# Performance work log

Measured on AMD Instinct MI355X. Metric: run time of the kernel, lower is better.

## Reference

```python
import jax, jax.numpy as jnp
import numpy as np

N_NODES = 500_000
N_EDGES = 16_000_000
GCN_DIMS = [1, 4, 7, 10, 16]   # gcn layer in/out widths
MLP_DIMS = [16, 32, 16, 16]    # fc1, fc2, fc3 (raw_feature_size=16)


def setup_inputs() -> dict:
    key = jax.random.key(0)
    ks = list(jax.random.split(key, 40))
    ki = iter(ks)
    inp = {}
    inp["x"] = jax.random.normal(next(ki), (N_NODES, 1), dtype=jnp.float32)
    inp["edge_index"] = jax.random.randint(next(ki), (2, N_EDGES), 0, N_NODES, dtype=jnp.int32)
    # GraphConv params: lin_rel (weight+bias) applied to aggregated neighbors,
    # lin_root (weight, no bias) applied to self features.
    for li in range(4):
        din, dout = GCN_DIMS[li], GCN_DIMS[li + 1]
        s = 1.0 / np.sqrt(din)
        inp[f"g{li+1}_Wrel"] = jax.random.uniform(next(ki), (din, dout), jnp.float32, -s, s)
        inp[f"g{li+1}_brel"] = jax.random.uniform(next(ki), (dout,), jnp.float32, -s, s)
        inp[f"g{li+1}_Wroot"] = jax.random.uniform(next(ki), (din, dout), jnp.float32, -s, s)
    for li in range(3):
        din, dout = MLP_DIMS[li], MLP_DIMS[li + 1]
        s = 1.0 / np.sqrt(din)
        inp[f"fc{li+1}_W"] = jax.random.uniform(next(ki), (din, dout), jnp.float32, -s, s)
        inp[f"fc{li+1}_b"] = jax.random.uniform(next(ki), (dout,), jnp.float32, -s, s)
    return inp


def _graph_conv(x, Wrel, brel, Wroot, src, dst):
    # PyG GraphConv, aggr='add': out_i = Wrel @ (sum_{j->i} x_j) + brel + Wroot @ x_i
    agg = jax.ops.segment_sum(x[src], dst, num_segments=N_NODES)  # [N, din]
    return agg @ Wrel + brel + x @ Wroot


def reference(x, edge_index,
              g1_Wrel, g1_brel, g1_Wroot,
              g2_Wrel, g2_brel, g2_Wroot,
              g3_Wrel, g3_brel, g3_Wroot,
              g4_Wrel, g4_brel, g4_Wroot,
              fc1_W, fc1_b, fc2_W, fc2_b, fc3_W, fc3_b):
    src, dst = edge_index[0], edge_index[1]
    h = jax.nn.relu(_graph_conv(x, g1_Wrel, g1_brel, g1_Wroot, src, dst))
    h = jax.nn.relu(_graph_conv(h, g2_Wrel, g2_brel, g2_Wroot, src, dst))
    h = jax.nn.relu(_graph_conv(h, g3_Wrel, g3_brel, g3_Wroot, src, dst))
    h = jax.nn.relu(_graph_conv(h, g4_Wrel, g4_brel, g4_Wroot, src, dst))
    h = jax.nn.relu(h @ fc1_W + fc1_b)
    h = jax.nn.relu(h @ fc2_W + fc2_b)
    return h @ fc3_W + fc3_b
```

## Files before the change

### kernel.cpp

```cpp
#include <hip/hip_runtime.h>
#include <hip/hip_fp16.h>

#define N_NODES 500000
#define N_EDGES 16000000

#define SB_BITS 13
#define SB_SIZE (1 << SB_BITS)
#define NSUPER ((N_NODES + SB_SIZE - 1) / SB_SIZE)
#define CAP1 270336
#define BKT_BITS 9
#define BKT_SIZE (1 << BKT_BITS)
#define NBUCKET ((N_NODES + BKT_SIZE - 1) / BKT_SIZE)
#define BKT_CAP 18432
#define B1_EPT 256
#define B1_CHUNK (256 * B1_EPT)
#define B1_NBLK ((N_EDGES + B1_CHUNK - 1) / B1_CHUNK)
#define B1_VQ (B1_EPT / 4)
#define NV4 (N_EDGES / 4)
#define B2_PER_SUPER 8

typedef unsigned int u32x2 __attribute__((ext_vector_type(2)));
typedef unsigned int u32x4 __attribute__((ext_vector_type(4)));
typedef float f32x2 __attribute__((ext_vector_type(2)));
typedef float f32x4 __attribute__((ext_vector_type(4)));

__device__ __forceinline__ unsigned int h2u(__half2 h) { return *(unsigned int*)&h; }
__device__ __forceinline__ float2 u2f2(unsigned int u) { return __half22float2(*(__half2*)&u); }

__global__ __launch_bounds__(512) void init_bcur_kernel(
    int* __restrict__ bcur1, int* __restrict__ bcur2)
{
    int i = blockIdx.x * 512 + threadIdx.x;
    if (i < NSUPER) bcur1[i] = i * CAP1;
    if (i < NBUCKET) bcur2[i] = i * BKT_CAP;
}

__global__ __launch_bounds__(256) void bin1_kernel(
    const int* __restrict__ src, const int* __restrict__ dst,
    int* __restrict__ bcur1, unsigned int* __restrict__ pairs1)
{
    __shared__ int lh[NSUPER];
    __shared__ int lbase[NSUPER];
    const int4* dst4 = (const int4*)dst;
    const int4* src4 = (const int4*)src;
    int t = threadIdx.x;
    long v0 = (long)blockIdx.x * (B1_CHUNK / 4);

    if (t < NSUPER) lh[t] = 0;
    __syncthreads();

#pragma unroll 8
    for (int q = 0; q < B1_VQ; ++q) {
        long v = v0 + q * 256 + t;
        if (v < NV4) {
            int4 d = dst4[v];
            atomicAdd(&lh[d.x >> SB_BITS], 1);
            atomicAdd(&lh[d.y >> SB_BITS], 1);
            atomicAdd(&lh[d.z >> SB_BITS], 1);
            atomicAdd(&lh[d.w >> SB_BITS], 1);
        }
    }
    __syncthreads();

    if (t < NSUPER) {
        int c = lh[t];
        lbase[t] = c ? atomicAdd(&bcur1[t], c) : 0;
        lh[t] = 0;
    }
    __syncthreads();

#pragma unroll 8
    for (int q = 0; q < B1_VQ; ++q) {
        long v = v0 + q * 256 + t;
        if (v < NV4) {
            int4 d = dst4[v];
            int4 s = src4[v];
            {
                int b = d.x >> SB_BITS;
                int r = atomicAdd(&lh[b], 1);
                pairs1[lbase[b] + r] = ((unsigned int)s.x << SB_BITS) | (unsigned int)(d.x & (SB_SIZE - 1));
            }
            {
                int b = d.y >> SB_BITS;
                int r = atomicAdd(&lh[b], 1);
                pairs1[lbase[b] + r] = ((unsigned int)s.y << SB_BITS) | (unsigned int)(d.y & (SB_SIZE - 1));
            }
            {
                int b = d.z >> SB_BITS;
                int r = atomicAdd(&lh[b], 1);
                pairs1[lbase[b] + r] = ((unsigned int)s.z << SB_BITS) | (unsigned int)(d.z & (SB_SIZE - 1));
            }
            {
                int b = d.w >> SB_BITS;
                int r = atomicAdd(&lh[b], 1);
                pairs1[lbase[b] + r] = ((unsigned int)s.w << SB_BITS) | (unsigned int)(d.w & (SB_SIZE - 1));
            }
        }
    }
}

__global__ __launch_bounds__(256) void bin2_kernel(
    const int* __restrict__ bcur1, int* __restrict__ bcur2,
    const unsigned int* __restrict__ pairs1, unsigned int* __restrict__ pairs2)
{
    __shared__ int lh[16];
    __shared__ int lbase[16];
    int s = blockIdx.x >> 3;
    int blk = blockIdx.x & 7;
    int t = threadIdx.x;
    int count = bcur1[s] - s * CAP1;
    int chunk = (((count + B2_PER_SUPER - 1) / B2_PER_SUPER) + 3) & ~3;
    int lo = blk * chunk;
    int hi = lo + chunk; if (hi > count) hi = count;
    int len = hi > lo ? hi - lo : 0;
    const unsigned int* base = pairs1 + (size_t)s * CAP1 + lo;
    const uint4* p4 = (const uint4*)base;
    int nv = len >> 2;

    if (t < 16) lh[t] = 0;
    __syncthreads();

    for (int i = t; i < nv; i += 256) {
        uint4 p = p4[i];
        atomicAdd(&lh[(p.x & (SB_SIZE - 1)) >> BKT_BITS], 1);
        atomicAdd(&lh[(p.y & (SB_SIZE - 1)) >> BKT_BITS], 1);
        atomicAdd(&lh[(p.z & (SB_SIZE - 1)) >> BKT_BITS], 1);
        atomicAdd(&lh[(p.w & (SB_SIZE - 1)) >> BKT_BITS], 1);
    }
    if (t < (len & 3))
        atomicAdd(&lh[(base[(nv << 2) + t] & (SB_SIZE - 1)) >> BKT_BITS], 1);
    __syncthreads();

    if (t < 16) {
        int c = lh[t];
        lbase[t] = c ? atomicAdd(&bcur2[(s << 4) | t], c) : 0;
        lh[t] = 0;
    }
    __syncthreads();

    for (int i = t; i < nv; i += 256) {
        uint4 p = p4[i];
#pragma unroll
        for (int q = 0; q < 4; ++q) {
            unsigned int e = (q == 0) ? p.x : (q == 1) ? p.y : (q == 2) ? p.z : p.w;
            int sub = (int)((e & (SB_SIZE - 1)) >> BKT_BITS);
            int r = atomicAdd(&lh[sub], 1);
            pairs2[lbase[sub] + r] = ((e >> SB_BITS) << BKT_BITS) | (e & (BKT_SIZE - 1));
        }
    }
    if (t < (len & 3)) {
        unsigned int e = base[(nv << 2) + t];
        int sub = (int)((e & (SB_SIZE - 1)) >> BKT_BITS);
        int r = atomicAdd(&lh[sub], 1);
        pairs2[lbase[sub] + r] = ((e >> SB_BITS) << BKT_BITS) | (e & (BKT_SIZE - 1));
    }
}

__global__ __launch_bounds__(512) void bucket_scan_kernel(
    const int* __restrict__ bcur2, int* __restrict__ bbase)
{
    __shared__ int sdata[512];
    int t = threadIdx.x;
    int i0 = t * 2;
    int v0 = (i0 < NBUCKET) ? (bcur2[i0] - i0 * BKT_CAP) : 0;
    int v1 = (i0 + 1 < NBUCKET) ? (bcur2[i0 + 1] - (i0 + 1) * BKT_CAP) : 0;
    int s = v0 + v1;
    sdata[t] = s;
    __syncthreads();
    for (int o = 1; o < 512; o <<= 1) {
        int tmp = (t >= o) ? sdata[t - o] : 0;
        __syncthreads();
        sdata[t] += tmp;
        __syncthreads();
    }
    int run = sdata[t] - s;
    if (i0 < NBUCKET) bbase[i0] = run;
    if (i0 + 1 < NBUCKET) bbase[i0 + 1] = run + v0;
    if (i0 == NBUCKET - 1) bbase[NBUCKET] = run + v0;
    if (i0 + 1 == NBUCKET - 1) bbase[NBUCKET] = run + v0 + v1;
}

__global__ __launch_bounds__(512) void bucket_sort512_kernel(
    const int* __restrict__ bcur2, const int* __restrict__ bbase,
    const unsigned int* __restrict__ pairs2, const float* __restrict__ xfeat,
    int* __restrict__ off, int* __restrict__ sorted_src,
    float* __restrict__ agg1)
{
    __shared__ int   stage[BKT_CAP];
    __shared__ int   lh[BKT_SIZE];
    __shared__ float laccum[BKT_SIZE];
    __shared__ int   sdata[512];
    int b = blockIdx.x;
    int t = threadIdx.x;
    int base_node = b << BKT_BITS;
    size_t pstart = (size_t)b * BKT_CAP;
    int count = bcur2[b] - b * BKT_CAP;
    int cstart = bbase[b];

    lh[t] = 0; laccum[t] = 0.0f;
    __syncthreads();

    int nv = count >> 2;
    const uint4* p4 = (const uint4*)(pairs2 + pstart);
    for (int i = t; i < nv; i += 512) {
        uint4 p = p4[i];
        atomicAdd(&lh[p.x & (BKT_SIZE - 1)], 1);
        atomicAdd(&lh[p.y & (BKT_SIZE - 1)], 1);
        atomicAdd(&lh[p.z & (BKT_SIZE - 1)], 1);
        atomicAdd(&lh[p.w & (BKT_SIZE - 1)], 1);
    }
    if (t < (count & 3))
        atomicAdd(&lh[pairs2[pstart + (nv << 2) + t] & (BKT_SIZE - 1)], 1);
    __syncthreads();

    int c = lh[t];
    sdata[t] = c;
    __syncthreads();
    for (int o = 1; o < 512; o <<= 1) {
        int tmp = (t >= o) ? sdata[t - o] : 0;
        __syncthreads();
        sdata[t] += tmp;
        __syncthreads();
    }
    int run = cstart + sdata[t] - c;
    int node = base_node + t;
    if (node < N_NODES) {
        off[node] = run;
        if (node == N_NODES - 1) off[N_NODES] = run + c;
    }
    lh[t] = run;
    __syncthreads();

    for (int i = t; i < nv; i += 512) {
        uint4 p = p4[i];
#pragma unroll
        for (int q = 0; q < 4; ++q) {
            unsigned int pe = (q == 0) ? p.x : (q == 1) ? p.y : (q == 2) ? p.z : p.w;
            int low = (int)(pe & (BKT_SIZE - 1));
            int sidx = (int)(pe >> BKT_BITS);
            int pos = atomicAdd(&lh[low], 1);
            stage[pos - cstart] = sidx;
            atomicAdd(&laccum[low], xfeat[sidx]);
        }
    }
    if (t < (count & 3)) {
        unsigned int pe = pairs2[pstart + (nv << 2) + t];
        int low = (int)(pe & (BKT_SIZE - 1));
        int sidx = (int)(pe >> BKT_BITS);
        int pos = atomicAdd(&lh[low], 1);
        stage[pos - cstart] = sidx;
        atomicAdd(&laccum[low], xfeat[sidx]);
    }
    __syncthreads();

    for (int j = t; j < count; j += 512)
        __builtin_nontemporal_store(stage[j], &sorted_src[cstart + j]);
    if (node < N_NODES) __builtin_nontemporal_store(laccum[t], &agg1[node]);
}

__global__ __launch_bounds__(256) void transform1_kernel(
    const float* __restrict__ agg1, const float* __restrict__ x,
    const float* __restrict__ Wrel, const float* __restrict__ brel,
    const float* __restrict__ Wroot,
    __half2* __restrict__ h1)
{
    __shared__ float w[12];
    if (threadIdx.x < 4) {
        w[threadIdx.x] = Wrel[threadIdx.x];
        w[4 + threadIdx.x] = brel[threadIdx.x];
        w[8 + threadIdx.x] = Wroot[threadIdx.x];
    }
    __syncthreads();
    int i = blockIdx.x * blockDim.x + threadIdx.x;
    if (i >= N_NODES) return;
    float a = agg1[i], xv = x[i];
    float r0 = fmaxf(a * w[0] + w[4] + xv * w[8],  0.0f);
    float r1 = fmaxf(a * w[1] + w[5] + xv * w[9],  0.0f);
    float r2 = fmaxf(a * w[2] + w[6] + xv * w[10], 0.0f);
    float r3 = fmaxf(a * w[3] + w[7] + xv * w[11], 0.0f);
    u32x2 v = { h2u(__floats2half2_rn(r0, r1)), h2u(__floats2half2_rn(r2, r3)) };
    __builtin_nontemporal_store(v, (u32x2*)(h1 + (size_t)i * 2));
}

__global__ __launch_bounds__(256) void gather2t_kernel(
    const int* __restrict__ off, const int* __restrict__ ss,
    const __half2* __restrict__ h1,
    const float* __restrict__ Wrel, const float* __restrict__ brel,
    const float* __restrict__ Wroot,
    __half2* __restrict__ h2)
{
    __shared__ float tile[128 * 5];
    __shared__ float sWr[28], sWo[28], sb[7];
    int t = threadIdx.x;
    if (t < 28) { sWr[t] = Wrel[t]; sWo[t] = Wroot[t]; }
    if (t < 7) sb[t] = brel[t];

    int ln = t >> 1;
    int j = t & 1;
    int node = blockIdx.x * 128 + ln;
    if (node < N_NODES) {
        int start = off[node], end = off[node + 1];
        float a0x=0,a0y=0,a1x=0,a1y=0,a2x=0,a2y=0,a3x=0,a3y=0;
        float b0x=0,b0y=0,b1x=0,b1y=0,b2x=0,b2y=0,b3x=0,b3y=0;
        int e = start;
        for (; e + 8 <= end; e += 8) {
            int s0=ss[e],s1=ss[e+1],s2=ss[e+2],s3=ss[e+3];
            int s4=ss[e+4],s5=ss[e+5],s6=ss[e+6],s7=ss[e+7];
            float2 f0=__half22float2(h1[(size_t)s0*2+j]);
            float2 f1=__half22float2(h1[(size_t)s1*2+j]);
            float2 f2=__half22float2(h1[(size_t)s2*2+j]);
            float2 f3=__half22float2(h1[(size_t)s3*2+j]);
            float2 f4=__half22float2(h1[(size_t)s4*2+j]);
            float2 f5=__half22float2(h1[(size_t)s5*2+j]);
            float2 f6=__half22float2(h1[(size_t)s6*2+j]);
            float2 f7=__half22float2(h1[(size_t)s7*2+j]);
            a0x+=f0.x;a0y+=f0.y; a1x+=f1.x;a1y+=f1.y;
            a2x+=f2.x;a2y+=f2.y; a3x+=f3.x;a3y+=f3.y;
            b0x+=f4.x;b0y+=f4.y; b1x+=f5.x;b1y+=f5.y;
            b2x+=f6.x;b2y+=f6.y; b3x+=f7.x;b3y+=f7.y;
        }
        for (; e < end; ++e) {
            float2 f = __half22float2(h1[(size_t)ss[e]*2+j]);
            a0x += f.x; a0y += f.y;
        }
        float rx = ((a0x+a1x)+(a2x+a3x)) + ((b0x+b1x)+(b2x+b3x));
        float ry = ((a0y+a1y)+(a2y+a3y)) + ((b0y+b1y)+(b2y+b3y));
        tile[ln * 5 + 2 * j] = rx;
        tile[ln * 5 + 2 * j + 1] = ry;
    }
    __syncthreads();

    if (t < 128) {
        int n2 = blockIdx.x * 128 + t;
        if (n2 < N_NODES) {
            float av[4];
#pragma unroll
            for (int k = 0; k < 4; ++k) av[k] = tile[t * 5 + k];
            float2 x01 = __half22float2(h1[(size_t)n2 * 2]);
            float2 x23 = __half22float2(h1[(size_t)n2 * 2 + 1]);
            float xv[4] = {x01.x, x01.y, x23.x, x23.y};
            float o_[8];
#pragma unroll
            for (int o = 0; o < 7; ++o) {
                float v = sb[o];
#pragma unroll
                for (int k = 0; k < 4; ++k)
                    v += av[k] * sWr[k * 7 + o] + xv[k] * sWo[k * 7 + o];
                o_[o] = fmaxf(v, 0.0f);
            }
            o_[7] = 0.0f;
            u32x4 v = { h2u(__floats2half2_rn(o_[0], o_[1])),
                        h2u(__floats2half2_rn(o_[2], o_[3])),
                        h2u(__floats2half2_rn(o_[4], o_[5])),
                        h2u(__floats2half2_rn(o_[6], o_[7])) };
            __builtin_nontemporal_store(v, (u32x4*)(h2 + (size_t)n2 * 4));
        }
    }
}

__global__ __launch_bounds__(256) void gather3t_kernel(
    const int* __restrict__ off, const int* __restrict__ ss,
    const __half2* __restrict__ h2,
    const float* __restrict__ Wrel, const float* __restrict__ brel,
    const float* __restrict__ Wroot,
    __half2* __restrict__ h3)
{
    __shared__ float tile[64 * 9];
    __shared__ float sWr[70], sWo[70], sb[10];
    int t = threadIdx.x;
    if (t < 70) { sWr[t] = Wrel[t]; sWo[t] = Wroot[t]; }
    if (t < 10) sb[t] = brel[t];

    int ln = t >> 2;
    int j = t & 3;
    int node = blockIdx.x * 64 + ln;
    if (node < N_NODES) {
        int start = off[node], end = off[node + 1];
        float a0x=0,a0y=0,a1x=0,a1y=0,a2x=0,a2y=0,a3x=0,a3y=0;
        float b0x=0,b0y=0,b1x=0,b1y=0,b2x=0,b2y=0,b3x=0,b3y=0;
        int e = start;
        for (; e + 8 <= end; e += 8) {
            int s0=ss[e],s1=ss[e+1],s2=ss[e+2],s3=ss[e+3];
            int s4=ss[e+4],s5=ss[e+5],s6=ss[e+6],s7=ss[e+7];
            float2 f0=__half22float2(h2[(size_t)s0*4+j]);
            float2 f1=__half22float2(h2[(size_t)s1*4+j]);
            float2 f2=__half22float2(h2[(size_t)s2*4+j]);
            float2 f3=__half22float2(h2[(size_t)s3*4+j]);
            float2 f4=__half22float2(h2[(size_t)s4*4+j]);
            float2 f5=__half22float2(h2[(size_t)s5*4+j]);
            float2 f6=__half22float2(h2[(size_t)s6*4+j]);
            float2 f7=__half22float2(h2[(size_t)s7*4+j]);
            a0x+=f0.x;a0y+=f0.y; a1x+=f1.x;a1y+=f1.y;
            a2x+=f2.x;a2y+=f2.y; a3x+=f3.x;a3y+=f3.y;
            b0x+=f4.x;b0y+=f4.y; b1x+=f5.x;b1y+=f5.y;
            b2x+=f6.x;b2y+=f6.y; b3x+=f7.x;b3y+=f7.y;
        }
        for (; e < end; ++e) {
            float2 f = __half22float2(h2[(size_t)ss[e]*4+j]);
            a0x += f.x; a0y += f.y;
        }
        float rx = ((a0x+a1x)+(a2x+a3x)) + ((b0x+b1x)+(b2x+b3x));
        float ry = ((a0y+a1y)+(a2y+a3y)) + ((b0y+b1y)+(b2y+b3y));
        tile[ln * 9 + 2 * j] = rx;
        tile[ln * 9 + 2 * j + 1] = ry;
    }
    __syncthreads();

    if (t < 64) {
        int n2 = blockIdx.x * 64 + t;
        if (n2 < N_NODES) {
            float av[7];
#pragma unroll
            for (int k = 0; k < 7; ++k) av[k] = tile[t * 9 + k];
            float xv[8];
#pragma unroll
            for (int q = 0; q < 4; ++q) {
                float2 f = __half22float2(h2[(size_t)n2 * 4 + q]);
                xv[2 * q] = f.x; xv[2 * q + 1] = f.y;
            }
            float o_[16];
#pragma unroll
            for (int o = 0; o < 10; ++o) {
                float v = sb[o];
#pragma unroll
                for (int k = 0; k < 7; ++k)
                    v += av[k] * sWr[k * 10 + o] + xv[k] * sWo[k * 10 + o];
                o_[o] = fmaxf(v, 0.0f);
            }
#pragma unroll
            for (int o = 10; o < 16; ++o) o_[o] = 0.0f;
            u32x4 v0 = { h2u(__floats2half2_rn(o_[0], o_[1])),
                         h2u(__floats2half2_rn(o_[2], o_[3])),
                         h2u(__floats2half2_rn(o_[4], o_[5])),
                         h2u(__floats2half2_rn(o_[6], o_[7])) };
            u32x4 v1 = { h2u(__floats2half2_rn(o_[8], o_[9])),
                         h2u(__floats2half2_rn(o_[10], o_[11])),
                         h2u(__floats2half2_rn(o_[12], o_[13])),
                         h2u(__floats2half2_rn(o_[14], o_[15])) };
            __builtin_nontemporal_store(v0, (u32x4*)(h3 + (size_t)n2 * 8));
            __builtin_nontemporal_store(v1, (u32x4*)(h3 + (size_t)n2 * 8 + 4));
        }
    }
}

__global__ __launch_bounds__(256) void gather4_kernel(
    const int* __restrict__ off, const int* __restrict__ ss,
    const __half2* __restrict__ h3, float* __restrict__ agg)
{
    int node = blockIdx.x * 32 + (threadIdx.x >> 3);
    int j = threadIdx.x & 7;
    if (node >= N_NODES) return;
    int start = off[node], end = off[node + 1];

    float a0x=0,a0y=0,a1x=0,a1y=0,a2x=0,a2y=0,a3x=0,a3y=0;
    float b0x=0,b0y=0,b1x=0,b1y=0,b2x=0,b2y=0,b3x=0,b3y=0;
    int e = start;
    for (; e + 16 <= end; e += 16) {
        int s0=ss[e+0], s1=ss[e+1], s2=ss[e+2],  s3=ss[e+3];
        int s4=ss[e+4], s5=ss[e+5], s6=ss[e+6],  s7=ss[e+7];
        int s8=ss[e+8], s9=ss[e+9], sa=ss[e+10], sb=ss[e+11];
        int sc=ss[e+12],sd=ss[e+13],se=ss[e+14], sf=ss[e+15];
        float2 f0=__half22float2(h3[(size_t)s0*8+j]);
        float2 f1=__half22float2(h3[(size_t)s1*8+j]);
        float2 f2=__half22float2(h3[(size_t)s2*8+j]);
        float2 f3=__half22float2(h3[(size_t)s3*8+j]);
        float2 f4=__half22float2(h3[(size_t)s4*8+j]);
        float2 f5=__half22float2(h3[(size_t)s5*8+j]);
        float2 f6=__half22float2(h3[(size_t)s6*8+j]);
        float2 f7=__half22float2(h3[(size_t)s7*8+j]);
        float2 f8=__half22float2(h3[(size_t)s8*8+j]);
        float2 f9=__half22float2(h3[(size_t)s9*8+j]);
        float2 fa=__half22float2(h3[(size_t)sa*8+j]);
        float2 fb=__half22float2(h3[(size_t)sb*8+j]);
        float2 fc=__half22float2(h3[(size_t)sc*8+j]);
        float2 fd=__half22float2(h3[(size_t)sd*8+j]);
        float2 fe=__half22float2(h3[(size_t)se*8+j]);
        float2 ff=__half22float2(h3[(size_t)sf*8+j]);
        a0x+=f0.x;a0y+=f0.y; a1x+=f1.x;a1y+=f1.y;
        a2x+=f2.x;a2y+=f2.y; a3x+=f3.x;a3y+=f3.y;
        b0x+=f4.x;b0y+=f4.y; b1x+=f5.x;b1y+=f5.y;
        b2x+=f6.x;b2y+=f6.y; b3x+=f7.x;b3y+=f7.y;
        a0x+=f8.x;a0y+=f8.y; a1x+=f9.x;a1y+=f9.y;
        a2x+=fa.x;a2y+=fa.y; a3x+=fb.x;a3y+=fb.y;
        b0x+=fc.x;b0y+=fc.y; b1x+=fd.x;b1y+=fd.y;
        b2x+=fe.x;b2y+=fe.y; b3x+=ff.x;b3y+=ff.y;
    }
    for (; e + 4 <= end; e += 4) {
        int s0=ss[e+0], s1=ss[e+1], s2=ss[e+2], s3=ss[e+3];
        float2 f0=__half22float2(h3[(size_t)s0*8+j]);
        float2 f1=__half22float2(h3[(size_t)s1*8+j]);
        float2 f2=__half22float2(h3[(size_t)s2*8+j]);
        float2 f3=__half22float2(h3[(size_t)s3*8+j]);
        a0x+=f0.x;a0y+=f0.y; a1x+=f1.x;a1y+=f1.y;
        a2x+=f2.x;a2y+=f2.y; a3x+=f3.x;a3y+=f3.y;
    }
    for (; e < end; ++e) {
        float2 f = __half22float2(h3[(size_t)ss[e]*8+j]);
        a0x += f.x; a0y += f.y;
    }
    float rx = ((a0x+a1x)+(a2x+a3x)) + ((b0x+b1x)+(b2x+b3x));
    float ry = ((a0y+a1y)+(a2y+a3y)) + ((b0y+b1y)+(b2y+b3y));
    f32x2 v = { rx, ry };
    __builtin_nontemporal_store(v, (f32x2*)(agg + (size_t)node * 16 + j * 2));
}

__global__ __launch_bounds__(256) void layer4_mlp_kernel(
    const float* __restrict__ agg, const __half2* __restrict__ h3,
    const float* __restrict__ g4Wrel, const float* __restrict__ g4brel,
    const float* __restrict__ g4Wroot,
    const float* __restrict__ fc1W, const float* __restrict__ fc1b,
    const float* __restrict__ fc2W, const float* __restrict__ fc2b,
    const float* __restrict__ fc3W, const float* __restrict__ fc3b,
    float* __restrict__ out)
{
    __shared__ float s[1680];
    float* sWrel  = s;
    float* sbrel  = s + 160;
    float* sWroot = s + 176;
    float* sfc1W  = s + 336;
    float* sfc1b  = s + 848;
    float* sfc2W  = s + 880;
    float* sfc2b  = s + 1392;
    float* sfc3W  = s + 1408;
    float* sfc3b  = s + 1664;
    int t = threadIdx.x;
    for (int i = t; i < 160; i += 256) { sWrel[i] = g4Wrel[i]; sWroot[i] = g4Wroot[i]; }
    for (int i = t; i < 512; i += 256) { sfc1W[i] = fc1W[i]; sfc2W[i] = fc2W[i]; }
    if (t < 256) sfc3W[t] = fc3W[t];
    if (t < 32)  sfc1b[t] = fc1b[t];
    if (t < 16)  { sbrel[t] = g4brel[t]; sfc2b[t] = fc2b[t]; sfc3b[t] = fc3b[t]; }
    __syncthreads();

    int i = blockIdx.x * blockDim.x + threadIdx.x;
    if (i >= N_NODES) return;

    const float4* ap = (const float4*)(agg + (size_t)i * 16);
    float4 a0 = ap[0], a1 = ap[1], a2 = ap[2];
    float a[10] = {a0.x, a0.y, a0.z, a0.w, a1.x, a1.y, a1.z, a1.w, a2.x, a2.y};
    float xin[10];
#pragma unroll
    for (int q = 0; q < 5; ++q) {
        float2 f = __half22float2(h3[(size_t)i * 8 + q]);
        xin[2 * q] = f.x; xin[2 * q + 1] = f.y;
    }

    float h4[16];
#pragma unroll
    for (int o = 0; o < 16; ++o) {
        float v = sbrel[o];
#pragma unroll
        for (int k = 0; k < 10; ++k)
            v += a[k] * sWrel[k * 16 + o] + xin[k] * sWroot[k * 16 + o];
        h4[o] = fmaxf(v, 0.0f);
    }
    float m1[32];
#pragma unroll
    for (int o = 0; o < 32; ++o) {
        float v = sfc1b[o];
#pragma unroll
        for (int k = 0; k < 16; ++k) v += h4[k] * sfc1W[k * 32 + o];
        m1[o] = fmaxf(v, 0.0f);
    }
    float m2[16];
#pragma unroll
    for (int o = 0; o < 16; ++o) {
        float v = sfc2b[o];
#pragma unroll
        for (int k = 0; k < 32; ++k) v += m1[k] * sfc2W[k * 16 + o];
        m2[o] = fmaxf(v, 0.0f);
    }
    float r[16];
#pragma unroll
    for (int o = 0; o < 16; ++o) {
        float v = sfc3b[o];
#pragma unroll
        for (int k = 0; k < 16; ++k) v += m2[k] * sfc3W[k * 16 + o];
        r[o] = v;
    }
#pragma unroll
    for (int q = 0; q < 4; ++q) {
        f32x4 v = { r[q*4+0], r[q*4+1], r[q*4+2], r[q*4+3] };
        __builtin_nontemporal_store(v, (f32x4*)(out + (size_t)i * 16 + q * 4));
    }
}

extern "C" void kernel_launch(void* const* d_in, const int* in_sizes, int n_in,
                              void* d_out, int out_size, void* d_ws, size_t ws_size,
                              hipStream_t stream) {
    const float* x        = (const float*)d_in[0];
    const int*   ei       = (const int*)d_in[1];
    const float* g1_Wrel  = (const float*)d_in[2];
    const float* g1_brel  = (const float*)d_in[3];
    const float* g1_Wroot = (const float*)d_in[4];
    const float* g2_Wrel  = (const float*)d_in[5];
    const float* g2_brel  = (const float*)d_in[6];
    const float* g2_Wroot = (const float*)d_in[7];
    const float* g3_Wrel  = (const float*)d_in[8];
    const float* g3_brel  = (const float*)d_in[9];
    const float* g3_Wroot = (const float*)d_in[10];
    const float* g4_Wrel  = (const float*)d_in[11];
    const float* g4_brel  = (const float*)d_in[12];
    const float* g4_Wroot = (const float*)d_in[13];
    const float* fc1_W    = (const float*)d_in[14];
    const float* fc1_b    = (const float*)d_in[15];
    const float* fc2_W    = (const float*)d_in[16];
    const float* fc2_b    = (const float*)d_in[17];
    const float* fc3_W    = (const float*)d_in[18];
    const float* fc3_b    = (const float*)d_in[19];
    float* out = (float*)d_out;

    const int* srcp = ei;
    const int* dstp = ei + N_EDGES;

    char* p = (char*)d_ws;
    auto alloc = [&](size_t bytes) {
        char* r = p;
        p += (bytes + 255) & ~(size_t)255;
        return r;
    };
    __half2* h1  = (__half2*)alloc((size_t)N_NODES * 4 * 2);
    __half2* h2  = (__half2*)alloc((size_t)N_NODES * 8 * 2);
    __half2* h3  = (__half2*)alloc((size_t)N_NODES * 16 * 2);
    float*   agg = (float*)  alloc((size_t)N_NODES * 16 * 4);
    alloc((size_t)14 * 1024 * 1024);
    unsigned int* pairs2 = (unsigned int*)h1;
    int* sorted_src = (int*)alloc((size_t)NSUPER * CAP1 * 4);
    unsigned int* pairs1 = (unsigned int*)sorted_src;
    int*   off   = (int*)alloc((size_t)(N_NODES + 1) * 4);
    float* agg1  = (float*)alloc((size_t)N_NODES * 4);
    int*   bcur1 = (int*)alloc((size_t)NSUPER * 4);
    int*   bcur2 = (int*)alloc((size_t)NBUCKET * 4);
    int*   bbase = (int*)alloc((size_t)(NBUCKET + 1) * 4);

    const int TB = 256;
    const int node_blocks = (N_NODES + TB - 1) / TB;

    init_bcur_kernel<<<2, 512, 0, stream>>>(bcur1, bcur2);
    bin1_kernel<<<B1_NBLK, 256, 0, stream>>>(srcp, dstp, bcur1, pairs1);
    bin2_kernel<<<NSUPER * B2_PER_SUPER, 256, 0, stream>>>(bcur1, bcur2, pairs1, pairs2);
    bucket_scan_kernel<<<1, 512, 0, stream>>>(bcur2, bbase);
    bucket_sort512_kernel<<<NBUCKET, 512, 0, stream>>>(
        bcur2, bbase, pairs2, x, off, sorted_src, agg1);

    transform1_kernel<<<node_blocks, TB, 0, stream>>>(
        agg1, x, g1_Wrel, g1_brel, g1_Wroot, h1);

    gather2t_kernel<<<(N_NODES + 127) / 128, TB, 0, stream>>>(
        off, sorted_src, h1, g2_Wrel, g2_brel, g2_Wroot, h2);
    gather3t_kernel<<<(N_NODES + 63) / 64, TB, 0, stream>>>(
        off, sorted_src, h2, g3_Wrel, g3_brel, g3_Wroot, h3);

    gather4_kernel<<<(N_NODES + 31) / 32, TB, 0, stream>>>(off, sorted_src, h3, agg);
    layer4_mlp_kernel<<<node_blocks, TB, 0, stream>>>(
        agg, h3, g4_Wrel, g4_brel, g4_Wroot,
        fc1_W, fc1_b, fc2_W, fc2_b, fc3_W, fc3_b, out);
}
```

Before: 878.7 us.

## Sub-sort each node's neighbors by source quarter and split layer-4 gather into four passes

```diff
diff --git a/kernel.cpp b/kernel.cpp
--- a/kernel.cpp
+++ b/kernel.cpp
@@ -11,7 +11,9 @@
 #define BKT_BITS 9
 #define BKT_SIZE (1 << BKT_BITS)
 #define NBUCKET ((N_NODES + BKT_SIZE - 1) / BKT_SIZE)
-#define BKT_CAP 18432
+#define BKT_CAP 17408
+#define QBITS 2
+#define NKEY (BKT_SIZE << QBITS)
 #define B1_EPT 256
 #define B1_CHUNK (256 * B1_EPT)
 #define B1_NBLK ((N_EDGES + B1_CHUNK - 1) / B1_CHUNK)
@@ -183,13 +185,12 @@
 __global__ __launch_bounds__(512) void bucket_sort512_kernel(
     const int* __restrict__ bcur2, const int* __restrict__ bbase,
     const unsigned int* __restrict__ pairs2, const float* __restrict__ xfeat,
-    int* __restrict__ off, int* __restrict__ sorted_src,
+    int* __restrict__ off4, int* __restrict__ sorted_src,
     float* __restrict__ agg1)
 {
     __shared__ int   stage[BKT_CAP];
-    __shared__ int   lh[BKT_SIZE];
+    __shared__ int   lh[NKEY];
     __shared__ float laccum[BKT_SIZE];
-    __shared__ int   sdata[512];
     int b = blockIdx.x;
     int t = threadIdx.x;
     int base_node = b << BKT_BITS;
@@ -197,38 +198,50 @@
     int count = bcur2[b] - b * BKT_CAP;
     int cstart = bbase[b];
 
-    lh[t] = 0; laccum[t] = 0.0f;
+    lh[t] = 0; lh[512 + t] = 0; lh[1024 + t] = 0; lh[1536 + t] = 0;
+    laccum[t & (BKT_SIZE - 1)] = 0.0f;
     __syncthreads();
 
     int nv = count >> 2;
     const uint4* p4 = (const uint4*)(pairs2 + pstart);
     for (int i = t; i < nv; i += 512) {
         uint4 p = p4[i];
-        atomicAdd(&lh[p.x & (BKT_SIZE - 1)], 1);
-        atomicAdd(&lh[p.y & (BKT_SIZE - 1)], 1);
-        atomicAdd(&lh[p.z & (BKT_SIZE - 1)], 1);
-        atomicAdd(&lh[p.w & (BKT_SIZE - 1)], 1);
-    }
-    if (t < (count & 3))
-        atomicAdd(&lh[pairs2[pstart + (nv << 2) + t] & (BKT_SIZE - 1)], 1);
-    __syncthreads();
-
-    int c = lh[t];
-    sdata[t] = c;
+        atomicAdd(&lh[((p.x & (BKT_SIZE - 1)) << QBITS) | (p.x >> 26)], 1);
+        atomicAdd(&lh[((p.y & (BKT_SIZE - 1)) << QBITS) | (p.y >> 26)], 1);
+        atomicAdd(&lh[((p.z & (BKT_SIZE - 1)) << QBITS) | (p.z >> 26)], 1);
+        atomicAdd(&lh[((p.w & (BKT_SIZE - 1)) << QBITS) | (p.w >> 26)], 1);
+    }
+    if (t < (count & 3)) {
+        unsigned int pe = pairs2[pstart + (nv << 2) + t];
+        atomicAdd(&lh[((pe & (BKT_SIZE - 1)) << QBITS) | (pe >> 26)], 1);
+    }
+    __syncthreads();
+
+    int i0 = t * 4;
+    int c0 = lh[i0], c1 = lh[i0 + 1], c2 = lh[i0 + 2], c3 = lh[i0 + 3];
+    int s = c0 + c1 + c2 + c3;
+    stage[t] = s;
     __syncthreads();
     for (int o = 1; o < 512; o <<= 1) {
-        int tmp = (t >= o) ? sdata[t - o] : 0;
+        int tmp = (t >= o) ? stage[t - o] : 0;
         __syncthreads();
-        sdata[t] += tmp;
+        stage[t] += tmp;
         __syncthreads();
     }
-    int run = cstart + sdata[t] - c;
-    int node = base_node + t;
-    if (node < N_NODES) {
-        off[node] = run;
-        if (node == N_NODES - 1) off[N_NODES] = run + c;
-    }
-    lh[t] = run;
+    int run = cstart + stage[t] - s;
+    int vals[4] = {c0, c1, c2, c3};
+#pragma unroll
+    for (int q = 0; q < 4; ++q) {
+        int key = i0 + q;
+        int node = base_node + (key >> QBITS);
+        if (node < N_NODES) {
+            off4[(size_t)base_node * 4 + key] = run;
+            if (node == N_NODES - 1 && (key & 3) == 3)
+                off4[(size_t)N_NODES * 4] = run + vals[q];
+        }
+        lh[key] = run;
+        run += vals[q];
+    }
     __syncthreads();
 
     for (int i = t; i < nv; i += 512) {
@@ -236,25 +249,26 @@
 #pragma unroll
         for (int q = 0; q < 4; ++q) {
             unsigned int pe = (q == 0) ? p.x : (q == 1) ? p.y : (q == 2) ? p.z : p.w;
-            int low = (int)(pe & (BKT_SIZE - 1));
+            int key = (int)(((pe & (BKT_SIZE - 1)) << QBITS) | (pe >> 26));
             int sidx = (int)(pe >> BKT_BITS);
-            int pos = atomicAdd(&lh[low], 1);
+            int pos = atomicAdd(&lh[key], 1);
             stage[pos - cstart] = sidx;
-            atomicAdd(&laccum[low], xfeat[sidx]);
+            atomicAdd(&laccum[pe & (BKT_SIZE - 1)], xfeat[sidx]);
         }
     }
     if (t < (count & 3)) {
         unsigned int pe = pairs2[pstart + (nv << 2) + t];
-        int low = (int)(pe & (BKT_SIZE - 1));
+        int key = (int)(((pe & (BKT_SIZE - 1)) << QBITS) | (pe >> 26));
         int sidx = (int)(pe >> BKT_BITS);
-        int pos = atomicAdd(&lh[low], 1);
+        int pos = atomicAdd(&lh[key], 1);
         stage[pos - cstart] = sidx;
-        atomicAdd(&laccum[low], xfeat[sidx]);
+        atomicAdd(&laccum[pe & (BKT_SIZE - 1)], xfeat[sidx]);
     }
     __syncthreads();
 
     for (int j = t; j < count; j += 512)
         __builtin_nontemporal_store(stage[j], &sorted_src[cstart + j]);
+    int node = base_node + t;
     if (node < N_NODES) __builtin_nontemporal_store(laccum[t], &agg1[node]);
 }
 
@@ -283,7 +297,7 @@
 }
 
 __global__ __launch_bounds__(256) void gather2t_kernel(
-    const int* __restrict__ off, const int* __restrict__ ss,
+    const int* __restrict__ off4, const int* __restrict__ ss,
     const __half2* __restrict__ h1,
     const float* __restrict__ Wrel, const float* __restrict__ brel,
     const float* __restrict__ Wroot,
@@ -299,7 +313,7 @@
     int j = t & 1;
     int node = blockIdx.x * 128 + ln;
     if (node < N_NODES) {
-        int start = off[node], end = off[node + 1];
+        int start = off4[(size_t)node * 4], end = off4[(size_t)node * 4 + 4];
         float a0x=0,a0y=0,a1x=0,a1y=0,a2x=0,a2y=0,a3x=0,a3y=0;
         float b0x=0,b0y=0,b1x=0,b1y=0,b2x=0,b2y=0,b3x=0,b3y=0;
         int e = start;
@@ -359,7 +373,7 @@
 }
 
 __global__ __launch_bounds__(256) void gather3t_kernel(
-    const int* __restrict__ off, const int* __restrict__ ss,
+    const int* __restrict__ off4, const int* __restrict__ ss,
     const __half2* __restrict__ h2,
     const float* __restrict__ Wrel, const float* __restrict__ brel,
     const float* __restrict__ Wroot,
@@ -375,7 +389,7 @@
     int j = t & 3;
     int node = blockIdx.x * 64 + ln;
     if (node < N_NODES) {
-        int start = off[node], end = off[node + 1];
+        int start = off4[(size_t)node * 4], end = off4[(size_t)node * 4 + 4];
         float a0x=0,a0y=0,a1x=0,a1y=0,a2x=0,a2y=0,a3x=0,a3y=0;
         float b0x=0,b0y=0,b1x=0,b1y=0,b2x=0,b2y=0,b3x=0,b3y=0;
         int e = start;
@@ -443,14 +457,15 @@
     }
 }
 
+template<int Q>
 __global__ __launch_bounds__(256) void gather4_kernel(
-    const int* __restrict__ off, const int* __restrict__ ss,
+    const int* __restrict__ off4, const int* __restrict__ ss,
     const __half2* __restrict__ h3, float* __restrict__ agg)
 {
     int node = blockIdx.x * 32 + (threadIdx.x >> 3);
     int j = threadIdx.x & 7;
     if (node >= N_NODES) return;
-    int start = off[node], end = off[node + 1];
+    int start = off4[(size_t)node * 4 + Q], end = off4[(size_t)node * 4 + Q + 1];
 
     float a0x=0,a0y=0,a1x=0,a1y=0,a2x=0,a2y=0,a3x=0,a3y=0;
     float b0x=0,b0y=0,b1x=0,b1y=0,b2x=0,b2y=0,b3x=0,b3y=0;
@@ -500,8 +515,15 @@
     }
     float rx = ((a0x+a1x)+(a2x+a3x)) + ((b0x+b1x)+(b2x+b3x));
     float ry = ((a0y+a1y)+(a2y+a3y)) + ((b0y+b1y)+(b2y+b3y));
-    f32x2 v = { rx, ry };
-    __builtin_nontemporal_store(v, (f32x2*)(agg + (size_t)node * 16 + j * 2));
+    float* dst = agg + (size_t)node * 16 + j * 2;
+    if (Q == 0) {
+        f32x2 v = { rx, ry };
+        __builtin_nontemporal_store(v, (f32x2*)dst);
+    } else {
+        f32x2 v = *(const f32x2*)dst;
+        v[0] += rx; v[1] += ry;
+        __builtin_nontemporal_store(v, (f32x2*)dst);
+    }
 }
 
 __global__ __launch_bounds__(256) void layer4_mlp_kernel(
@@ -618,15 +640,15 @@
         p += (bytes + 255) & ~(size_t)255;
         return r;
     };
-    __half2* h1  = (__half2*)alloc((size_t)N_NODES * 4 * 2);
-    __half2* h2  = (__half2*)alloc((size_t)N_NODES * 8 * 2);
-    __half2* h3  = (__half2*)alloc((size_t)N_NODES * 16 * 2);
+    __half2* h1  = (__half2*)alloc((size_t)N_NODES * 2 * sizeof(__half2));
+    __half2* h2  = (__half2*)alloc((size_t)N_NODES * 4 * sizeof(__half2));
+    __half2* h3  = (__half2*)alloc((size_t)N_NODES * 8 * sizeof(__half2));
     float*   agg = (float*)  alloc((size_t)N_NODES * 16 * 4);
     alloc((size_t)14 * 1024 * 1024);
     unsigned int* pairs2 = (unsigned int*)h1;
     int* sorted_src = (int*)alloc((size_t)NSUPER * CAP1 * 4);
     unsigned int* pairs1 = (unsigned int*)sorted_src;
-    int*   off   = (int*)alloc((size_t)(N_NODES + 1) * 4);
+    int*   off4  = (int*)alloc(((size_t)N_NODES * 4 + 1) * 4);
     float* agg1  = (float*)alloc((size_t)N_NODES * 4);
     int*   bcur1 = (int*)alloc((size_t)NSUPER * 4);
     int*   bcur2 = (int*)alloc((size_t)NBUCKET * 4);
@@ -640,17 +662,21 @@
     bin2_kernel<<<NSUPER * B2_PER_SUPER, 256, 0, stream>>>(bcur1, bcur2, pairs1, pairs2);
     bucket_scan_kernel<<<1, 512, 0, stream>>>(bcur2, bbase);
     bucket_sort512_kernel<<<NBUCKET, 512, 0, stream>>>(
-        bcur2, bbase, pairs2, x, off, sorted_src, agg1);
+        bcur2, bbase, pairs2, x, off4, sorted_src, agg1);
 
     transform1_kernel<<<node_blocks, TB, 0, stream>>>(
         agg1, x, g1_Wrel, g1_brel, g1_Wroot, h1);
 
     gather2t_kernel<<<(N_NODES + 127) / 128, TB, 0, stream>>>(
-        off, sorted_src, h1, g2_Wrel, g2_brel, g2_Wroot, h2);
+        off4, sorted_src, h1, g2_Wrel, g2_brel, g2_Wroot, h2);
     gather3t_kernel<<<(N_NODES + 63) / 64, TB, 0, stream>>>(
-        off, sorted_src, h2, g3_Wrel, g3_brel, g3_Wroot, h3);
-
-    gather4_kernel<<<(N_NODES + 31) / 32, TB, 0, stream>>>(off, sorted_src, h3, agg);
+        off4, sorted_src, h2, g3_Wrel, g3_brel, g3_Wroot, h3);
+
+    const int g4_blocks = (N_NODES + 31) / 32;
+    gather4_kernel<0><<<g4_blocks, TB, 0, stream>>>(off4, sorted_src, h3, agg);
+    gather4_kernel<1><<<g4_blocks, TB, 0, stream>>>(off4, sorted_src, h3, agg);
+    gather4_kernel<2><<<g4_blocks, TB, 0, stream>>>(off4, sorted_src, h3, agg);
+    gather4_kernel<3><<<g4_blocks, TB, 0, stream>>>(off4, sorted_src, h3, agg);
     layer4_mlp_kernel<<<node_blocks, TB, 0, stream>>>(
         agg, h3, g4_Wrel, g4_brel, g4_Wroot,
         fc1_W, fc1_b, fc2_W, fc2_b, fc3_W, fc3_b, out);
```

After: 877.5 us. No clear change (-0.1%).
